# Kernel optimization log

Hardware: AMD Instinct MI355X
Metric: run time of the kernel (lower is better)

The kernel has to match this reference:

```python
import jax, jax.numpy as jnp
import numpy as np

BN_EPS = 1e-4  # KAIR BatchNorm2d eps


def conv1x1(x, W, b):
    # x: (b,c,h,w), W: (out,in), b: (out,)
    return jnp.einsum('oc,bchw->bohw', W, x) + b[None, :, None, None]


def setup_inputs() -> dict:
    key = jax.random.key(0)
    ks = jax.random.split(key, 16)
    b, c, h, w = 8, 64, 128, 128
    f32 = jnp.float32

    def rn(k, shape, s=0.05):
        return jax.random.normal(k, shape, f32) * s

    c3 = 3 * c
    return {
        'x': jax.random.normal(ks[0], (b, c, h, w), f32),
        'xf': jax.random.normal(ks[1], (b, c, h, w), f32),
        'xr': jax.random.normal(ks[2], (b, c, h, w), f32),
        'Wx': rn(ks[3], (c, c)), 'bx': jnp.zeros((c,), f32),
        'Wx1': rn(ks[4], (c, c)), 'bx1': jnp.zeros((c,), f32),
        'Wx2': rn(ks[5], (c, c)), 'bx2': jnp.zeros((c,), f32),
        'Wxf': rn(ks[6], (c, c)), 'bxf': jnp.zeros((c,), f32),
        'Wxr': rn(ks[7], (c, c)), 'bxr': jnp.zeros((c,), f32),
        'W_msa': rn(ks[8], (c3, c3, 3, 3)), 'b_msa': jnp.zeros((c3,), f32),
        'bn_gamma': jnp.ones((c3,), f32), 'bn_beta': jnp.zeros((c3,), f32),
        'bn_mean': jnp.zeros((c3,), f32), 'bn_var': jnp.ones((c3,), f32),
    }


def reference(x, xf, xr, Wx, bx, Wx1, bx1, Wx2, bx2, Wxf, bxf, Wxr, bxr,
              W_msa, b_msa, bn_gamma, bn_beta, bn_mean, bn_var):
    x_org = x
    # 1x1 conv projections (note: x1/x2 are projections of the projected x)
    xp = conv1x1(x, Wx, bx)
    x1 = conv1x1(xp, Wx1, bx1)
    x2 = conv1x1(xp, Wx2, bx2)
    xfp = conv1x1(xf, Wxf, bxf)
    xrp = conv1x1(xr, Wxr, bxr)

    # score1 = rearrange(x1,'b c h w->b h c w') @ rearrange(xf,'b c h w->b h w c') -> (b,h,c,c)
    score1 = jnp.einsum('bchw,bdhw->bhcd', x1, xfp)
    # feature_xf = score1 @ rearrange(x,'b c h w->b h c w'), rearranged back to (b,c,h,w)
    feature_xf = jnp.einsum('bhcd,bdhw->bchw', score1, xp)
    score2 = jnp.einsum('bchw,bdhw->bhcd', x2, xrp)
    feature_xr = jnp.einsum('bhcd,bdhw->bchw', score2, xp)

    out = jnp.concatenate([feature_xf, feature_xr, x_org], axis=1)  # (b,3c,h,w)
    # msa_conv: Conv2d(3c,3c,3,s=1,p=1) + BatchNorm2d(eval) + ReLU
    out = jax.lax.conv_general_dilated(
        out, W_msa, window_strides=(1, 1), padding='SAME',
        dimension_numbers=('NCHW', 'OIHW', 'NCHW'))
    out = out + b_msa[None, :, None, None]
    inv = jax.lax.rsqrt(bn_var + BN_EPS)
    out = (out - bn_mean[None, :, None, None]) * (bn_gamma * inv)[None, :, None, None] \
          + bn_beta[None, :, None, None]
    return jax.nn.relu(out)
```

## Files before the change

### kernel.cpp

```cpp
#include <hip/hip_runtime.h>

#define BATCH 8
#define C     64
#define H     128
#define WD    128
#define C3    192
#define HW    (H*WD)
#define PW    130
#define ICS   192
#define CBUF  (4*PW*64)

#define SWZ(r) ((((r) & 7) ^ (((r) >> 3) & 6)))

typedef __attribute__((ext_vector_type(8))) short short8;
typedef __attribute__((ext_vector_type(4))) float f32x4;
typedef unsigned short ushort_t;

__device__ __forceinline__ unsigned short f2bf(float f) {
    unsigned u = __builtin_bit_cast(unsigned, f);
    u += 0x7fffu + ((u >> 16) & 1u);
    return (unsigned short)(u >> 16);
}
__device__ __forceinline__ int pack2(unsigned short lo, unsigned short hi) {
    return (int)(((unsigned)hi << 16) | (unsigned)lo);
}

__global__ __launch_bounds__(64) void compose_kernel(
    const float* __restrict__ Wx,  const float* __restrict__ bx,
    const float* __restrict__ Wx1, const float* __restrict__ bx1,
    const float* __restrict__ Wx2, const float* __restrict__ bx2,
    const float* __restrict__ Wxf, const float* __restrict__ bxf,
    const float* __restrict__ Wxr, const float* __restrict__ bxr,
    ushort_t* __restrict__ Wall, float* __restrict__ ball)
{
    int o = blockIdx.x;
    int c = threadIdx.x;
    Wall[0*4096 + o*64 + c] = f2bf(Wx [o*64 + c]);
    Wall[3*4096 + o*64 + c] = f2bf(Wxf[o*64 + c]);
    Wall[4*4096 + o*64 + c] = f2bf(Wxr[o*64 + c]);
    float a1 = 0.f, a2 = 0.f;
    for (int k = 0; k < 64; ++k) {
        float wc = Wx[k*64 + c];
        a1 += Wx1[o*64 + k] * wc;
        a2 += Wx2[o*64 + k] * wc;
    }
    Wall[1*4096 + o*64 + c] = f2bf(a1);
    Wall[2*4096 + o*64 + c] = f2bf(a2);
    float t1 = Wx1[o*64 + c] * bx[c];
    float t2 = Wx2[o*64 + c] * bx[c];
    for (int off = 32; off; off >>= 1) {
        t1 += __shfl_down(t1, off);
        t2 += __shfl_down(t2, off);
    }
    if (c == 0) {
        ball[0*64 + o] = bx[o];
        ball[1*64 + o] = bx1[o] + t1;
        ball[2*64 + o] = bx2[o] + t2;
        ball[3*64 + o] = bxf[o];
        ball[4*64 + o] = bxr[o];
    }
}

__global__ __launch_bounds__(256, 4) void attn_mfma(
    const float* __restrict__ xf, const float* __restrict__ xr,
    const ushort_t* __restrict__ Wall, const float* __restrict__ ball,
    ushort_t* inT2)
{
    __shared__ ushort_t lds[4*4096];
    ushort_t* P = lds;
    ushort_t* Q = lds + 4096;
    ushort_t* R = lds + 2*4096;
    ushort_t* T = lds + 3*4096;

    const int t = threadIdx.x;
    const int wv = t >> 6, lane = t & 63, m = lane & 15, quad = lane >> 4;
    const int b = blockIdx.x >> 7, h = blockIdx.x & 127;
    const float* xfs = xf + (size_t)b*C*HW + (size_t)h*WD;
    const float* xrs = xr + (size_t)b*C*HW + (size_t)h*WD;
    const size_t rowbase = ((size_t)b*PW + h + 1)*PW;

    auto stageX = [&](ushort_t* dst, int wc) {
#pragma unroll
        for (int it = 0; it < 2; ++it) {
            int slot = it*256 + t;
            int w = slot >> 3, seg = slot & 7;
            const ushort_t* src = inT2 + (rowbase + (wc + 1 + w))*ICS + 128 + seg*8;
            *(int4*)(dst + w*64 + ((seg ^ SWZ(w)) << 3)) = *(const int4*)src;
        }
    };
    auto stageF = [&](const float* src, int wc, ushort_t* dst) {
        int c = t >> 2, wq = (t & 3) << 4;
        const float* p = src + (size_t)c*HW + wc + wq;
        float4 v0 = *(const float4*)(p);
        float4 v1 = *(const float4*)(p + 4);
        float4 v2 = *(const float4*)(p + 8);
        float4 v3 = *(const float4*)(p + 12);
        float vv[16] = {v0.x,v0.y,v0.z,v0.w, v1.x,v1.y,v1.z,v1.w,
                        v2.x,v2.y,v2.z,v2.w, v3.x,v3.y,v3.z,v3.w};
        int cg = c >> 3, cl = c & 7;
#pragma unroll
        for (int j = 0; j < 16; ++j) {
            int row = wq + j;
            dst[row*64 + ((cg ^ SWZ(row)) << 3) + cl] = f2bf(vv[j]);
        }
    };
    auto projB = [&](const ushort_t* src, const ushort_t* W, const float* bias,
                     ushort_t* dst) {
        int mt = wv;
        int arow = mt*16 + m;
        int sa = SWZ(arow);
#pragma unroll
        for (int nt = 0; nt < 4; ++nt) {
            f32x4 acc = {0.f,0.f,0.f,0.f};
#pragma unroll
            for (int k = 0; k < 2; ++k) {
                short8 a  = *(const short8*)(src + arow*64 + (((4*k+quad) ^ sa) << 3));
                short8 bb = *(const short8*)(W   + (nt*16 + m)*64  + k*32 + quad*8);
                acc = __builtin_amdgcn_mfma_f32_16x16x32_bf16(a, bb, acc, 0,0,0);
            }
            float bo = bias[nt*16 + m];
            int o = nt*16 + m, w0 = mt*16 + quad*4;
            int base = o*64 + (((w0 >> 3) ^ SWZ(o)) << 3) + (w0 & 7);
            *(int*)(dst + base)     = pack2(f2bf(acc[0]+bo), f2bf(acc[1]+bo));
            *(int*)(dst + base + 2) = pack2(f2bf(acc[2]+bo), f2bf(acc[3]+bo));
        }
    };
    auto projA = [&](const ushort_t* src, const ushort_t* W, const float* bias,
                     ushort_t* dstT) {
        int mt = wv;
        float b4[4];
#pragma unroll
        for (int r = 0; r < 4; ++r) b4[r] = bias[mt*16 + quad*4 + r];
#pragma unroll
        for (int nt = 0; nt < 4; ++nt) {
            f32x4 acc = {0.f,0.f,0.f,0.f};
            int brow = nt*16 + m;
            int sb = SWZ(brow);
#pragma unroll
            for (int k = 0; k < 2; ++k) {
                short8 a  = *(const short8*)(W   + (mt*16 + m)*64  + k*32 + quad*8);
                short8 bb = *(const short8*)(src + brow*64 + (((4*k+quad) ^ sb) << 3));
                acc = __builtin_amdgcn_mfma_f32_16x16x32_bf16(a, bb, acc, 0,0,0);
            }
            int w = nt*16 + m, o0 = mt*16 + quad*4;
            int base = w*64 + (((o0 >> 3) ^ SWZ(w)) << 3) + (o0 & 7);
            *(int*)(dstT + base)     = pack2(f2bf(acc[0]+b4[0]), f2bf(acc[1]+b4[1]));
            *(int*)(dstT + base + 2) = pack2(f2bf(acc[2]+b4[2]), f2bf(acc[3]+b4[3]));
        }
    };
    auto scoreStep = [&](const ushort_t* A, const ushort_t* B, f32x4* sc) {
        int mt = wv;
        int arow = mt*16 + m;
        int sa = SWZ(arow);
#pragma unroll
        for (int nt = 0; nt < 4; ++nt) {
            int brow = nt*16 + m;
            int sb = SWZ(brow);
#pragma unroll
            for (int k = 0; k < 2; ++k) {
                short8 a  = *(const short8*)(A + arow*64 + (((4*k+quad) ^ sa) << 3));
                short8 bb = *(const short8*)(B + brow*64 + (((4*k+quad) ^ sb) << 3));
                sc[nt] = __builtin_amdgcn_mfma_f32_16x16x32_bf16(a, bb, sc[nt], 0,0,0);
            }
        }
    };
    auto scoreDump = [&](const f32x4* sc, ushort_t* dst) {
        int c0 = wv*16 + quad*4;
#pragma unroll
        for (int nt = 0; nt < 4; ++nt) {
            int d = nt*16 + m;
            int gd = d >> 3, dl = d & 7;
#pragma unroll
            for (int r = 0; r < 4; ++r) {
                int row = c0 + r;
                dst[row*64 + ((gd ^ SWZ(row)) << 3) + dl] = f2bf(sc[nt][r]);
            }
        }
    };
    auto feat = [&](const ushort_t* Sc, const ushort_t* XpT, ushort_t* stg) {
        int mt = wv;
        int arow = mt*16 + m;
        int sa = SWZ(arow);
#pragma unroll
        for (int nt = 0; nt < 4; ++nt) {
            f32x4 acc = {0.f,0.f,0.f,0.f};
            int brow = nt*16 + m;
            int sb = SWZ(brow);
#pragma unroll
            for (int k = 0; k < 2; ++k) {
                short8 a  = *(const short8*)(Sc  + arow*64 + (((4*k+quad) ^ sa) << 3));
                short8 bb = *(const short8*)(XpT + brow*64 + (((4*k+quad) ^ sb) << 3));
                acc = __builtin_amdgcn_mfma_f32_16x16x32_bf16(a, bb, acc, 0,0,0);
            }
            int w = nt*16 + m, c0 = mt*16 + quad*4;
            int base = w*64 + (((c0 >> 3) ^ SWZ(w)) << 3) + (c0 & 7);
            *(int*)(stg + base)     = pack2(f2bf(acc[0]), f2bf(acc[1]));
            *(int*)(stg + base + 2) = pack2(f2bf(acc[2]), f2bf(acc[3]));
        }
    };
    auto emitBr = [&](const ushort_t* stg, int wc, int coff) {
#pragma unroll
        for (int it = 0; it < 2; ++it) {
            int j = it*256 + t;
            int row = j >> 3, seg = j & 7;
            int4 v = *(const int4*)(stg + row*64 + ((seg ^ SWZ(row)) << 3));
            ushort_t* dst = inT2 + (rowbase + (wc + 1 + row))*ICS + coff + seg*8;
            *(int4*)dst = v;
        }
    };

    const ushort_t* W0 = Wall;            const float* b0 = ball;
    const ushort_t* W1 = Wall + 4096;     const float* b1 = ball + 64;
    const ushort_t* W2 = Wall + 2*4096;   const float* b2 = ball + 128;
    const ushort_t* W3 = Wall + 3*4096;   const float* b3 = ball + 192;
    const ushort_t* W4 = Wall + 4*4096;   const float* b4 = ball + 256;

    f32x4 sc1[4], sc2[4];
#pragma unroll
    for (int i = 0; i < 4; ++i) { sc1[i] = (f32x4){0,0,0,0}; sc2[i] = (f32x4){0,0,0,0}; }

    stageX(P, 0); stageF(xfs, 0, Q);
    __syncthreads();
    for (int wc = 0; wc < WD; wc += 64) {
        projB(P, W1, b1, R);  projB(Q, W3, b3, T);
        __syncthreads();
        scoreStep(R, T, sc1); stageF(xrs, wc, Q);
        __syncthreads();
        projB(P, W2, b2, R);  projB(Q, W4, b4, T);
        __syncthreads();
        scoreStep(R, T, sc2);
        if (wc == 0) { stageX(P, 64); stageF(xfs, 64, Q); }
        __syncthreads();
    }

    scoreDump(sc1, P);  scoreDump(sc2, R);  stageX(Q, 0);
    __syncthreads();
    int pp = 0;
    for (int wc = 0; wc < WD; wc += 64, pp ^= 1) {
        ushort_t* X  = pp ? T : Q;
        ushort_t* XT = pp ? Q : T;
        projA(X, W0, b0, XT);
        __syncthreads();
        feat(P, XT, X);
        __syncthreads();
        emitBr(X, wc, 0);
        __syncthreads();
        feat(R, XT, X);
        __syncthreads();
        emitBr(X, wc, 64);
        if (wc == 0) stageX(T, 64);
        __syncthreads();
    }
}

__global__ __launch_bounds__(256) void prep_kernel(const float* __restrict__ x,
                                                   ushort_t* __restrict__ inT2)
{
    int b  = blockIdx.x / PW, py = blockIdx.x % PW;
    int t  = threadIdx.x;
    ushort_t* rowp = inT2 + ((size_t)b*PW + py)*(size_t)PW*ICS;

    if (py == 0 || py == PW-1) {
        int4 z = make_int4(0,0,0,0);
        for (int j = t; j < PW*ICS/8; j += 256) ((int4*)rowp)[j] = z;
        return;
    }
    if (t < 48) {
        int side = t / 24, seg = t % 24;
        ((int4*)(rowp + (size_t)(side ? (PW-1) : 0)*ICS))[seg] = make_int4(0,0,0,0);
    }
    __shared__ ushort_t sx[128*72];
    int y = py - 1;
    for (int k = t; k < 64*128; k += 256) {
        int c = k >> 7, xx = k & 127;
        sx[xx*72 + c] = f2bf(x[((size_t)b*C + c)*HW + (size_t)y*WD + xx]);
    }
    __syncthreads();
    for (int j = t; j < 128*8; j += 256) {
        int xx = j >> 3, seg = j & 7;
        *(int4*)(rowp + (size_t)(xx+1)*ICS + 128 + seg*8) = *(const int4*)(sx + xx*72 + seg*8);
    }
}

__global__ __launch_bounds__(256) void pack_kernel(const float* __restrict__ W,
                                                   ushort_t* __restrict__ Wpk)
{
    int k = blockIdx.x*256 + threadIdx.x;
    if (k >= 12*54*64) return;
    int lane = k & 63, os = k >> 6;
    int otile = os / 54, s = os % 54;
    int tap = s / 6, icc = s % 6;
    int o   = otile*16 + (lane & 15);
    int ic0 = icc*32 + (lane >> 4)*8;
    ushort_t v[8];
#pragma unroll
    for (int j = 0; j < 8; ++j)
        v[j] = f2bf(W[(size_t)(o*C3 + ic0 + j)*9 + tap]);
    *(int4*)(Wpk + (size_t)k*8) = *(const int4*)v;
}

__global__ __launch_bounds__(512, 2) void conv_mfma(
    const ushort_t* __restrict__ inT2, const ushort_t* __restrict__ Wpk,
    const float* __restrict__ bias, const float* __restrict__ gamma,
    const float* __restrict__ beta, const float* __restrict__ mean,
    const float* __restrict__ var,  float* __restrict__ out)
{
    __shared__ ushort_t sA[2*CBUF];

    const int t = threadIdx.x;
    const int wv = t >> 6, lane = t & 63;
    const int m = lane & 15, quad = lane >> 4;
    const int b  = blockIdx.x >> 6, y0 = (blockIdx.x & 63)*2;
    const int yi = wv & 1, og = wv >> 1;

    f32x4 acc[32];
#pragma unroll
    for (int i = 0; i < 32; ++i) acc[i] = (f32x4){0.f,0.f,0.f,0.f};

    auto produce = [&](int ch, int bufi) {
        ushort_t* dst = sA + bufi*CBUF;
        const int ic0 = ch*64;
        const int pt = t - 384;
        for (int i = 0; i < 32; ++i) {
            int sl = i*128 + pt;
            int wi = sl & 7, rowgx = sl >> 3;
            int row = rowgx / PW, gx = rowgx - row*PW;
            int wl = wi ^ (gx & 7);
            const ushort_t* g = inT2 + (((size_t)b*PW + y0 + row)*PW + gx)*ICS
                                     + ic0 + wl*8;
            __builtin_amdgcn_global_load_lds(
                (const __attribute__((address_space(1))) unsigned int*)g,
                (__attribute__((address_space(3))) unsigned int*)(dst + (size_t)sl*8),
                16, 0, 0);
        }
        if (pt < 64) {
            int sl = 4096 + pt;
            int wi = sl & 7, rowgx = sl >> 3;
            int row = rowgx / PW, gx = rowgx - row*PW;
            int wl = wi ^ (gx & 7);
            const ushort_t* g = inT2 + (((size_t)b*PW + y0 + row)*PW + gx)*ICS
                                     + ic0 + wl*8;
            __builtin_amdgcn_global_load_lds(
                (const __attribute__((address_space(1))) unsigned int*)g,
                (__attribute__((address_space(3))) unsigned int*)(dst + (size_t)sl*8),
                16, 0, 0);
        }
    };

    auto compute = [&](int ch, int bufi) {
        const ushort_t* src = sA + bufi*CBUF;
        short8 bf[8], bfn[8];
#pragma unroll
        for (int j = 0; j < 4; ++j)
#pragma unroll
            for (int k = 0; k < 2; ++k)
                bf[j*2+k] = *(const short8*)(Wpk +
                    (((size_t)(og*4+j)*54 + ch*2 + k)*64 + lane)*8);
#pragma unroll
        for (int tap = 0; tap < 9; ++tap) {
            if (tap < 8) {
#pragma unroll
                for (int j = 0; j < 4; ++j)
#pragma unroll
                    for (int k = 0; k < 2; ++k)
                        bfn[j*2+k] = *(const short8*)(Wpk +
                            (((size_t)(og*4+j)*54 + (tap+1)*6 + ch*2 + k)*64 + lane)*8);
            }
            const int ky = tap/3, kx = tap - ky*3;
            const int sw = (kx + m) & 7;
            const int rowb = ((yi + ky)*PW + kx + m)*64;
            const int g0 = (quad ^ sw)*8, g1 = ((quad+4) ^ sw)*8;
#pragma unroll
            for (int xt = 0; xt < 8; ++xt) {
                short8 af0 = *(const short8*)(src + rowb + xt*1024 + g0);
                short8 af1 = *(const short8*)(src + rowb + xt*1024 + g1);
#pragma unroll
                for (int j = 0; j < 4; ++j) {
                    acc[j*8+xt] = __builtin_amdgcn_mfma_f32_16x16x32_bf16(af0, bf[j*2],   acc[j*8+xt], 0,0,0);
                    acc[j*8+xt] = __builtin_amdgcn_mfma_f32_16x16x32_bf16(af1, bf[j*2+1], acc[j*8+xt], 0,0,0);
                }
            }
#pragma unroll
            for (int q = 0; q < 8; ++q) bf[q] = bfn[q];
        }
    };

    if (wv >= 6) produce(0, 0);
    __syncthreads();
    for (int ch = 0; ch < 3; ++ch) {
        if (wv >= 6) { if (ch < 2) produce(ch + 1, (ch + 1) & 1); }
        else          compute(ch, ch & 1);
        __syncthreads();
    }

    float* sOut = (float*)sA;
    for (int y = 0; y < 2; ++y) {
        if (wv < 6 && yi == y) {
#pragma unroll
            for (int j = 0; j < 4; ++j) {
                int o = (og*4 + j)*16 + m;
                float A  = gamma[o] * rsqrtf(var[o] + 1e-4f);
                float Bv = (bias[o] - mean[o])*A + beta[o];
#pragma unroll
                for (int xt = 0; xt < 8; ++xt) {
                    f32x4 a4 = acc[j*8 + xt];
                    *(float4*)(sOut + o*132 + xt*16 + quad*4) =
                        make_float4(fmaxf(a4[0]*A + Bv, 0.f), fmaxf(a4[1]*A + Bv, 0.f),
                                    fmaxf(a4[2]*A + Bv, 0.f), fmaxf(a4[3]*A + Bv, 0.f));
                }
            }
        }
        __syncthreads();
#pragma unroll
        for (int i = 0; i < 12; ++i) {
            int s = i*512 + t;
            int o = s >> 5, xs4 = (s & 31)*4;
            float4 v = *(const float4*)(sOut + o*132 + xs4);
            *(float4*)(out + (((size_t)b*C3 + o)*H + y0 + y)*WD + xs4) = v;
        }
        __syncthreads();
    }
}

extern "C" void kernel_launch(void* const* d_in, const int* in_sizes, int n_in,
                              void* d_out, int out_size, void* d_ws, size_t ws_size,
                              hipStream_t stream)
{
    const float* x   = (const float*)d_in[0];
    const float* xf  = (const float*)d_in[1];
    const float* xr  = (const float*)d_in[2];
    const float* Wx  = (const float*)d_in[3];
    const float* bx  = (const float*)d_in[4];
    const float* Wx1 = (const float*)d_in[5];
    const float* bx1 = (const float*)d_in[6];
    const float* Wx2 = (const float*)d_in[7];
    const float* bx2 = (const float*)d_in[8];
    const float* Wxf = (const float*)d_in[9];
    const float* bxf = (const float*)d_in[10];
    const float* Wxr = (const float*)d_in[11];
    const float* bxr = (const float*)d_in[12];
    const float* Wm  = (const float*)d_in[13];
    const float* bms = (const float*)d_in[14];
    const float* gam = (const float*)d_in[15];
    const float* bet = (const float*)d_in[16];
    const float* mea = (const float*)d_in[17];
    const float* va  = (const float*)d_in[18];
    (void)in_sizes; (void)n_in; (void)out_size; (void)ws_size;

    ushort_t* inT2 = (ushort_t*)d_ws;
    ushort_t* Wpk  = (ushort_t*)((char*)d_ws + 52000000);
    ushort_t* Wall = (ushort_t*)((char*)d_ws + 52700000);
    float*    ball = (float*)   ((char*)d_ws + 52750000);
    float* outp = (float*)d_out;

    compose_kernel<<<dim3(64), dim3(64), 0, stream>>>(
        Wx, bx, Wx1, bx1, Wx2, bx2, Wxf, bxf, Wxr, bxr, Wall, ball);
    pack_kernel<<<dim3(162), dim3(256), 0, stream>>>(Wm, Wpk);
    prep_kernel<<<dim3(BATCH*PW), dim3(256), 0, stream>>>(x, inT2);
    attn_mfma<<<dim3(BATCH*H), dim3(256), 0, stream>>>(
        xf, xr, Wall, ball, inT2);
    conv_mfma<<<dim3(BATCH*64), dim3(512), 0, stream>>>(
        inT2, Wpk, bms, gam, bet, mea, va, outp);
}
```

Baseline: 398.7 us.

## Pre-transpose xf/xr to bf16 channel-last and split padded buffer into feat/xcl

The prep kernel now also converts xf and xr to bf16 channels-last, staging them in the output buffer as scratch, so the attention kernel loads them with plain vector copies instead of strided fp32 loads and per-element swizzled stores. The single 192-channel padded buffer is split into a 128-channel feature buffer and a 64-channel x buffer, and the conv producer picks the source per channel chunk. The attention kernel is restructured with six LDS tiles so both projections and scores are computed in a straight-line sequence with fewer barriers, at the cost of more LDS and a lower occupancy bound (3 blocks). Prep now writes extra bf16 copies of xf and xr that attention must read back, adding global traffic.

```diff
diff --git a/kernel.cpp b/kernel.cpp
--- a/kernel.cpp
+++ b/kernel.cpp
@@ -7,7 +7,6 @@
 #define C3    192
 #define HW    (H*WD)
 #define PW    130
-#define ICS   192
 #define CBUF  (4*PW*64)
 
 #define SWZ(r) ((((r) & 7) ^ (((r) >> 3) & 6)))
@@ -61,53 +60,100 @@
     }
 }
 
-__global__ __launch_bounds__(256, 4) void attn_mfma(
-    const float* __restrict__ xf, const float* __restrict__ xr,
+__global__ __launch_bounds__(256) void prep_kernel(
+    const float* __restrict__ x, const float* __restrict__ xf,
+    const float* __restrict__ xr,
+    ushort_t* __restrict__ xcl, ushort_t* __restrict__ feat,
+    ushort_t* __restrict__ xfT, ushort_t* __restrict__ xrT)
+{
+    int b  = blockIdx.x / PW, py = blockIdx.x % PW;
+    int t  = threadIdx.x;
+    const size_t prow = ((size_t)b*PW + py)*PW;
+
+    if (py == 0 || py == PW-1) {
+        int4 z = make_int4(0,0,0,0);
+        for (int j = t; j < PW*128/8; j += 256) ((int4*)(feat + prow*128))[j] = z;
+        for (int j = t; j < PW*64/8;  j += 256) ((int4*)(xcl  + prow*64 ))[j] = z;
+        return;
+    }
+    if (t < 48) {
+        int4 z = make_int4(0,0,0,0);
+        if (t < 32) {
+            int side = t >> 4, seg = t & 15;
+            *(int4*)(feat + (prow + (side ? PW-1 : 0))*128 + seg*8) = z;
+        } else {
+            int u = t - 32, side = u >> 3, seg = u & 7;
+            *(int4*)(xcl + (prow + (side ? PW-1 : 0))*64 + seg*8) = z;
+        }
+    }
+    __shared__ ushort_t sx[128*72];
+    const int y = py - 1;
+
+    for (int k = t; k < 64*128; k += 256) {
+        int c = k >> 7, xx = k & 127;
+        sx[xx*72 + c] = f2bf(x[((size_t)b*C + c)*HW + (size_t)y*WD + xx]);
+    }
+    __syncthreads();
+    for (int j = t; j < 128*8; j += 256) {
+        int xx = j >> 3, seg = j & 7;
+        *(int4*)(xcl + (prow + xx + 1)*64 + seg*8) = *(const int4*)(sx + xx*72 + seg*8);
+    }
+    __syncthreads();
+    for (int k = t; k < 64*128; k += 256) {
+        int c = k >> 7, xx = k & 127;
+        sx[xx*72 + c] = f2bf(xf[((size_t)b*C + c)*HW + (size_t)y*WD + xx]);
+    }
+    __syncthreads();
+    for (int j = t; j < 128*8; j += 256) {
+        int xx = j >> 3, seg = j & 7;
+        *(int4*)(xfT + (((size_t)b*128 + y)*128 + xx)*64 + seg*8) = *(const int4*)(sx + xx*72 + seg*8);
+    }
+    __syncthreads();
+    for (int k = t; k < 64*128; k += 256) {
+        int c = k >> 7, xx = k & 127;
+        sx[xx*72 + c] = f2bf(xr[((size_t)b*C + c)*HW + (size_t)y*WD + xx]);
+    }
+    __syncthreads();
+    for (int j = t; j < 128*8; j += 256) {
+        int xx = j >> 3, seg = j & 7;
+        *(int4*)(xrT + (((size_t)b*128 + y)*128 + xx)*64 + seg*8) = *(const int4*)(sx + xx*72 + seg*8);
+    }
+}
+
+__global__ __launch_bounds__(256, 3) void attn_mfma(
+    const ushort_t* __restrict__ xcl, const ushort_t* __restrict__ xfT,
+    const ushort_t* __restrict__ xrT,
     const ushort_t* __restrict__ Wall, const float* __restrict__ ball,
-    ushort_t* inT2)
-{
-    __shared__ ushort_t lds[4*4096];
+    ushort_t* __restrict__ feat)
+{
+    __shared__ ushort_t lds[6*4096];
     ushort_t* P = lds;
     ushort_t* Q = lds + 4096;
-    ushort_t* R = lds + 2*4096;
-    ushort_t* T = lds + 3*4096;
+    ushort_t* U = lds + 2*4096;
+    ushort_t* R = lds + 3*4096;
+    ushort_t* V = lds + 4*4096;
+    ushort_t* T = lds + 5*4096;
 
     const int t = threadIdx.x;
     const int wv = t >> 6, lane = t & 63, m = lane & 15, quad = lane >> 4;
     const int b = blockIdx.x >> 7, h = blockIdx.x & 127;
-    const float* xfs = xf + (size_t)b*C*HW + (size_t)h*WD;
-    const float* xrs = xr + (size_t)b*C*HW + (size_t)h*WD;
     const size_t rowbase = ((size_t)b*PW + h + 1)*PW;
-
-    auto stageX = [&](ushort_t* dst, int wc) {
+    const ushort_t* xrow  = xcl + (rowbase + 1)*64;
+    const ushort_t* xfrow = xfT + ((size_t)b*128 + h)*128*64;
+    const ushort_t* xrrow = xrT + ((size_t)b*128 + h)*128*64;
+
+    auto stageT = [&](const ushort_t* base, ushort_t* dst) {
 #pragma unroll
         for (int it = 0; it < 2; ++it) {
             int slot = it*256 + t;
             int w = slot >> 3, seg = slot & 7;
-            const ushort_t* src = inT2 + (rowbase + (wc + 1 + w))*ICS + 128 + seg*8;
-            *(int4*)(dst + w*64 + ((seg ^ SWZ(w)) << 3)) = *(const int4*)src;
-        }
-    };
-    auto stageF = [&](const float* src, int wc, ushort_t* dst) {
-        int c = t >> 2, wq = (t & 3) << 4;
-        const float* p = src + (size_t)c*HW + wc + wq;
-        float4 v0 = *(const float4*)(p);
-        float4 v1 = *(const float4*)(p + 4);
-        float4 v2 = *(const float4*)(p + 8);
-        float4 v3 = *(const float4*)(p + 12);
-        float vv[16] = {v0.x,v0.y,v0.z,v0.w, v1.x,v1.y,v1.z,v1.w,
-                        v2.x,v2.y,v2.z,v2.w, v3.x,v3.y,v3.z,v3.w};
-        int cg = c >> 3, cl = c & 7;
-#pragma unroll
-        for (int j = 0; j < 16; ++j) {
-            int row = wq + j;
-            dst[row*64 + ((cg ^ SWZ(row)) << 3) + cl] = f2bf(vv[j]);
+            *(int4*)(dst + w*64 + ((seg ^ SWZ(w)) << 3)) =
+                *(const int4*)(base + w*64 + seg*8);
         }
     };
     auto projB = [&](const ushort_t* src, const ushort_t* W, const float* bias,
                      ushort_t* dst) {
-        int mt = wv;
-        int arow = mt*16 + m;
+        int arow = wv*16 + m;
         int sa = SWZ(arow);
 #pragma unroll
         for (int nt = 0; nt < 4; ++nt) {
@@ -119,7 +165,7 @@
                 acc = __builtin_amdgcn_mfma_f32_16x16x32_bf16(a, bb, acc, 0,0,0);
             }
             float bo = bias[nt*16 + m];
-            int o = nt*16 + m, w0 = mt*16 + quad*4;
+            int o = nt*16 + m, w0 = wv*16 + quad*4;
             int base = o*64 + (((w0 >> 3) ^ SWZ(o)) << 3) + (w0 & 7);
             *(int*)(dst + base)     = pack2(f2bf(acc[0]+bo), f2bf(acc[1]+bo));
             *(int*)(dst + base + 2) = pack2(f2bf(acc[2]+bo), f2bf(acc[3]+bo));
@@ -127,10 +173,9 @@
     };
     auto projA = [&](const ushort_t* src, const ushort_t* W, const float* bias,
                      ushort_t* dstT) {
-        int mt = wv;
         float b4[4];
 #pragma unroll
-        for (int r = 0; r < 4; ++r) b4[r] = bias[mt*16 + quad*4 + r];
+        for (int r = 0; r < 4; ++r) b4[r] = bias[wv*16 + quad*4 + r];
 #pragma unroll
         for (int nt = 0; nt < 4; ++nt) {
             f32x4 acc = {0.f,0.f,0.f,0.f};
@@ -138,19 +183,18 @@
             int sb = SWZ(brow);
 #pragma unroll
             for (int k = 0; k < 2; ++k) {
-                short8 a  = *(const short8*)(W   + (mt*16 + m)*64  + k*32 + quad*8);
+                short8 a  = *(const short8*)(W   + (wv*16 + m)*64  + k*32 + quad*8);
                 short8 bb = *(const short8*)(src + brow*64 + (((4*k+quad) ^ sb) << 3));
                 acc = __builtin_amdgcn_mfma_f32_16x16x32_bf16(a, bb, acc, 0,0,0);
             }
-            int w = nt*16 + m, o0 = mt*16 + quad*4;
+            int w = nt*16 + m, o0 = wv*16 + quad*4;
             int base = w*64 + (((o0 >> 3) ^ SWZ(w)) << 3) + (o0 & 7);
             *(int*)(dstT + base)     = pack2(f2bf(acc[0]+b4[0]), f2bf(acc[1]+b4[1]));
             *(int*)(dstT + base + 2) = pack2(f2bf(acc[2]+b4[2]), f2bf(acc[3]+b4[3]));
         }
     };
     auto scoreStep = [&](const ushort_t* A, const ushort_t* B, f32x4* sc) {
-        int mt = wv;
-        int arow = mt*16 + m;
+        int arow = wv*16 + m;
         int sa = SWZ(arow);
 #pragma unroll
         for (int nt = 0; nt < 4; ++nt) {
@@ -177,9 +221,8 @@
             }
         }
     };
-    auto feat = [&](const ushort_t* Sc, const ushort_t* XpT, ushort_t* stg) {
-        int mt = wv;
-        int arow = mt*16 + m;
+    auto featF = [&](const ushort_t* Sc, const ushort_t* XpT, ushort_t* stg) {
+        int arow = wv*16 + m;
         int sa = SWZ(arow);
 #pragma unroll
         for (int nt = 0; nt < 4; ++nt) {
@@ -192,20 +235,21 @@
                 short8 bb = *(const short8*)(XpT + brow*64 + (((4*k+quad) ^ sb) << 3));
                 acc = __builtin_amdgcn_mfma_f32_16x16x32_bf16(a, bb, acc, 0,0,0);
             }
-            int w = nt*16 + m, c0 = mt*16 + quad*4;
+            int w = nt*16 + m, c0 = wv*16 + quad*4;
             int base = w*64 + (((c0 >> 3) ^ SWZ(w)) << 3) + (c0 & 7);
             *(int*)(stg + base)     = pack2(f2bf(acc[0]), f2bf(acc[1]));
             *(int*)(stg + base + 2) = pack2(f2bf(acc[2]), f2bf(acc[3]));
         }
     };
-    auto emitBr = [&](const ushort_t* stg, int wc, int coff) {
-#pragma unroll
-        for (int it = 0; it < 2; ++it) {
-            int j = it*256 + t;
+    auto emitPair = [&](const ushort_t* O1, const ushort_t* O2, int wc) {
+#pragma unroll
+        for (int it = 0; it < 4; ++it) {
+            int j = (it & 1)*256 + t;
+            const ushort_t* S = (it < 2) ? O1 : O2;
+            int half = (it < 2) ? 0 : 64;
             int row = j >> 3, seg = j & 7;
-            int4 v = *(const int4*)(stg + row*64 + ((seg ^ SWZ(row)) << 3));
-            ushort_t* dst = inT2 + (rowbase + (wc + 1 + row))*ICS + coff + seg*8;
-            *(int4*)dst = v;
+            int4 v = *(const int4*)(S + row*64 + ((seg ^ SWZ(row)) << 3));
+            *(int4*)(feat + (rowbase + wc + 1 + row)*128 + half + seg*8) = v;
         }
     };
 
@@ -219,67 +263,36 @@
 #pragma unroll
     for (int i = 0; i < 4; ++i) { sc1[i] = (f32x4){0,0,0,0}; sc2[i] = (f32x4){0,0,0,0}; }
 
-    stageX(P, 0); stageF(xfs, 0, Q);
-    __syncthreads();
-    for (int wc = 0; wc < WD; wc += 64) {
-        projB(P, W1, b1, R);  projB(Q, W3, b3, T);
-        __syncthreads();
-        scoreStep(R, T, sc1); stageF(xrs, wc, Q);
-        __syncthreads();
-        projB(P, W2, b2, R);  projB(Q, W4, b4, T);
-        __syncthreads();
-        scoreStep(R, T, sc2);
-        if (wc == 0) { stageX(P, 64); stageF(xfs, 64, Q); }
-        __syncthreads();
-    }
-
-    scoreDump(sc1, P);  scoreDump(sc2, R);  stageX(Q, 0);
-    __syncthreads();
-    int pp = 0;
-    for (int wc = 0; wc < WD; wc += 64, pp ^= 1) {
-        ushort_t* X  = pp ? T : Q;
-        ushort_t* XT = pp ? Q : T;
-        projA(X, W0, b0, XT);
-        __syncthreads();
-        feat(P, XT, X);
-        __syncthreads();
-        emitBr(X, wc, 0);
-        __syncthreads();
-        feat(R, XT, X);
-        __syncthreads();
-        emitBr(X, wc, 64);
-        if (wc == 0) stageX(T, 64);
-        __syncthreads();
-    }
-}
-
-__global__ __launch_bounds__(256) void prep_kernel(const float* __restrict__ x,
-                                                   ushort_t* __restrict__ inT2)
-{
-    int b  = blockIdx.x / PW, py = blockIdx.x % PW;
-    int t  = threadIdx.x;
-    ushort_t* rowp = inT2 + ((size_t)b*PW + py)*(size_t)PW*ICS;
-
-    if (py == 0 || py == PW-1) {
-        int4 z = make_int4(0,0,0,0);
-        for (int j = t; j < PW*ICS/8; j += 256) ((int4*)rowp)[j] = z;
-        return;
-    }
-    if (t < 48) {
-        int side = t / 24, seg = t % 24;
-        ((int4*)(rowp + (size_t)(side ? (PW-1) : 0)*ICS))[seg] = make_int4(0,0,0,0);
-    }
-    __shared__ ushort_t sx[128*72];
-    int y = py - 1;
-    for (int k = t; k < 64*128; k += 256) {
-        int c = k >> 7, xx = k & 127;
-        sx[xx*72 + c] = f2bf(x[((size_t)b*C + c)*HW + (size_t)y*WD + xx]);
-    }
-    __syncthreads();
-    for (int j = t; j < 128*8; j += 256) {
-        int xx = j >> 3, seg = j & 7;
-        *(int4*)(rowp + (size_t)(xx+1)*ICS + 128 + seg*8) = *(const int4*)(sx + xx*72 + seg*8);
-    }
+    stageT(xrow, P); stageT(xfrow, Q); stageT(xrrow, U);
+    __syncthreads();
+    projB(P, W1, b1, R);  projB(P, W2, b2, V);  projB(Q, W3, b3, T);
+    __syncthreads();
+    scoreStep(R, T, sc1); projB(U, W4, b4, Q);
+    __syncthreads();
+    scoreStep(V, Q, sc2);
+    stageT(xrow + 64*64, P); stageT(xfrow + 64*64, T); stageT(xrrow + 64*64, U);
+    __syncthreads();
+    projB(P, W1, b1, R);  projB(P, W2, b2, V);  projB(T, W3, b3, Q);
+    __syncthreads();
+    scoreStep(R, Q, sc1); projB(U, W4, b4, T);
+    __syncthreads();
+    scoreStep(V, T, sc2);
+    stageT(xrow, P);
+    __syncthreads();
+
+    scoreDump(sc1, Q);  scoreDump(sc2, U);
+    __syncthreads();
+    projA(P, W0, b0, R);
+    __syncthreads();
+    featF(Q, R, P);  featF(U, R, T);  stageT(xrow + 64*64, V);
+    __syncthreads();
+    emitPair(P, T, 0);
+    __syncthreads();
+    projA(V, W0, b0, R);
+    __syncthreads();
+    featF(Q, R, V);  featF(U, R, T);
+    __syncthreads();
+    emitPair(V, T, 64);
 }
 
 __global__ __launch_bounds__(256) void pack_kernel(const float* __restrict__ W,
@@ -300,7 +313,8 @@
 }
 
 __global__ __launch_bounds__(512, 2) void conv_mfma(
-    const ushort_t* __restrict__ inT2, const ushort_t* __restrict__ Wpk,
+    const ushort_t* __restrict__ feat, const ushort_t* __restrict__ xcl,
+    const ushort_t* __restrict__ Wpk,
     const float* __restrict__ bias, const float* __restrict__ gamma,
     const float* __restrict__ beta, const float* __restrict__ mean,
     const float* __restrict__ var,  float* __restrict__ out)
@@ -319,15 +333,17 @@
 
     auto produce = [&](int ch, int bufi) {
         ushort_t* dst = sA + bufi*CBUF;
-        const int ic0 = ch*64;
+        const ushort_t* base = (ch < 2) ? feat : xcl;
+        const int ps = (ch < 2) ? 128 : 64;
+        const int co = (ch == 1) ? 64 : 0;
         const int pt = t - 384;
         for (int i = 0; i < 32; ++i) {
             int sl = i*128 + pt;
             int wi = sl & 7, rowgx = sl >> 3;
             int row = rowgx / PW, gx = rowgx - row*PW;
             int wl = wi ^ (gx & 7);
-            const ushort_t* g = inT2 + (((size_t)b*PW + y0 + row)*PW + gx)*ICS
-                                     + ic0 + wl*8;
+            const ushort_t* g = base + (((size_t)b*PW + y0 + row)*PW + gx)*ps
+                                     + co + wl*8;
             __builtin_amdgcn_global_load_lds(
                 (const __attribute__((address_space(1))) unsigned int*)g,
                 (__attribute__((address_space(3))) unsigned int*)(dst + (size_t)sl*8),
@@ -338,8 +354,8 @@
             int wi = sl & 7, rowgx = sl >> 3;
             int row = rowgx / PW, gx = rowgx - row*PW;
             int wl = wi ^ (gx & 7);
-            const ushort_t* g = inT2 + (((size_t)b*PW + y0 + row)*PW + gx)*ICS
-                                     + ic0 + wl*8;
+            const ushort_t* g = base + (((size_t)b*PW + y0 + row)*PW + gx)*ps
+                                     + co + wl*8;
             __builtin_amdgcn_global_load_lds(
                 (const __attribute__((address_space(1))) unsigned int*)g,
                 (__attribute__((address_space(3))) unsigned int*)(dst + (size_t)sl*8),
@@ -447,18 +463,22 @@
     const float* va  = (const float*)d_in[18];
     (void)in_sizes; (void)n_in; (void)out_size; (void)ws_size;
 
-    ushort_t* inT2 = (ushort_t*)d_ws;
-    ushort_t* Wpk  = (ushort_t*)((char*)d_ws + 52000000);
+    ushort_t* feat = (ushort_t*)d_ws;
+    ushort_t* xcl  = (ushort_t*)((char*)d_ws + 34611200);
+    ushort_t* Wpk  = (ushort_t*)((char*)d_ws + 51916800);
     ushort_t* Wall = (ushort_t*)((char*)d_ws + 52700000);
     float*    ball = (float*)   ((char*)d_ws + 52750000);
+    ushort_t* xfT  = (ushort_t*)d_out;
+    ushort_t* xrT  = (ushort_t*)((char*)d_out + 16777216);
     float* outp = (float*)d_out;
 
     compose_kernel<<<dim3(64), dim3(64), 0, stream>>>(
         Wx, bx, Wx1, bx1, Wx2, bx2, Wxf, bxf, Wxr, bxr, Wall, ball);
     pack_kernel<<<dim3(162), dim3(256), 0, stream>>>(Wm, Wpk);
-    prep_kernel<<<dim3(BATCH*PW), dim3(256), 0, stream>>>(x, inT2);
+    prep_kernel<<<dim3(BATCH*PW), dim3(256), 0, stream>>>(
+        x, xf, xr, xcl, feat, xfT, xrT);
     attn_mfma<<<dim3(BATCH*H), dim3(256), 0, stream>>>(
-        xf, xr, Wall, ball, inT2);
+        xcl, xfT, xrT, Wall, ball, feat);
     conv_mfma<<<dim3(BATCH*64), dim3(512), 0, stream>>>(
-        inT2, Wpk, bms, gam, bet, mea, va, outp);
-}
+        feat, xcl, Wpk, bms, gam, bet, mea, va, outp);
+}
```

Measured after the change: 371.5 us. -6.8%, faster.
